# Kernel tuning notes

Hardware: AMD Instinct MI355X
Metric: run time of the kernel (lower is better)

The kernel has to match this reference:

```python
import jax, jax.numpy as jnp
import numpy as np

EPS = 1e-8  # matches torch F.cosine_similarity eps


def setup_inputs() -> dict:
    key = jax.random.key(0)
    S, U, D = 2048, 10, 256  # speakers, utterances/speaker, embedding dim
    embeddings = jax.random.normal(key, (S * U, D), dtype=jnp.float32)
    labels = jnp.repeat(jnp.arange(S, dtype=jnp.int64), U)  # speaker-blocked, as the view() assumes
    return {"embeddings": embeddings, "labels": labels}


def reference(embeddings, labels):
    labels_np = np.asarray(labels)
    S = int(np.unique(labels_np).size)          # num_speakers (static)
    B, D = embeddings.shape
    U = B // S                                   # num_utterances
    E = embeddings.reshape(S, U, D)
    C = E.mean(axis=1)                           # (S, D) centroids
    En = E / jnp.maximum(jnp.linalg.norm(E, axis=-1, keepdims=True), EPS)
    Cn = C / jnp.maximum(jnp.linalg.norm(C, axis=-1, keepdims=True), EPS)
    sim = jnp.einsum('sud,kd->suk', En, Cn)      # (S, U, S) cosine similarities
    idx = jnp.arange(S)
    pos = sim[idx, :, idx]                       # (S, U) similarity to own centroid
    neg_mask = jnp.eye(S, dtype=bool)[:, None, :]  # mask out k == i
    neg = jnp.where(neg_mask, -jnp.inf, sim)
    lse = jax.nn.logsumexp(neg, axis=-1)         # (S, U)
    loss = jnp.mean(-pos + lse)
    return loss
```

## Files before the change

### kernel.cpp

```cpp
#include <hip/hip_runtime.h>
#include <math.h>

#define SS   2048
#define UU   10
#define DD   256
#define BB   (SS * UU)
#define EPSF 1e-8f

typedef __attribute__((ext_vector_type(8))) short   bf16x8;
typedef __attribute__((ext_vector_type(4))) float   floatx4;

__device__ static inline unsigned short f2bf(float f) {
    union { float f; unsigned u; } v; v.f = f;
    unsigned r = (v.u + 0x7FFFu + ((v.u >> 16) & 1u)) >> 16;
    return (unsigned short)r;
}

__device__ static inline void gl_lds16(const unsigned short* g, unsigned short* l) {
    __builtin_amdgcn_global_load_lds((const __attribute__((address_space(1))) void*)g,
                                     (__attribute__((address_space(3))) void*)l, 16, 0, 0);
}

__global__ __launch_bounds__(256) void prep_kernel(const float* __restrict__ E,
                                                   unsigned short* __restrict__ Enb,
                                                   unsigned short* __restrict__ Cnb,
                                                   float* __restrict__ sumexp,
                                                   float* __restrict__ out) {
    const int s   = blockIdx.x;
    const int wid = threadIdx.x >> 6, lane = threadIdx.x & 63;
    __shared__ float cent[4][256];
    __shared__ float sred[256];

    if (threadIdx.x < UU) sumexp[s * UU + threadIdx.x] = 0.f;
    if (s == 0 && threadIdx.x == 0) out[0] = 0.f;

    float cp0 = 0.f, cp1 = 0.f, cp2 = 0.f, cp3 = 0.f;
    for (int u = wid; u < UU; u += 4) {
        const size_t roff = (size_t)(s * UU + u) * DD;
        float4 v = ((const float4*)(E + roff))[lane];
        float ssq = v.x * v.x + v.y * v.y + v.z * v.z + v.w * v.w;
#pragma unroll
        for (int off = 32; off; off >>= 1) ssq += __shfl_xor(ssq, off, 64);
        const float rinv = 1.0f / fmaxf(sqrtf(ssq), EPSF);
        ushort4 o;
        o.x = f2bf(v.x * rinv); o.y = f2bf(v.y * rinv);
        o.z = f2bf(v.z * rinv); o.w = f2bf(v.w * rinv);
        ((ushort4*)(Enb + roff))[lane] = o;
        cp0 += v.x; cp1 += v.y; cp2 += v.z; cp3 += v.w;
    }
    cent[wid][lane * 4 + 0] = cp0;
    cent[wid][lane * 4 + 1] = cp1;
    cent[wid][lane * 4 + 2] = cp2;
    cent[wid][lane * 4 + 3] = cp3;
    __syncthreads();

    const int d = threadIdx.x;
    const float c = (cent[0][d] + cent[1][d] + cent[2][d] + cent[3][d]) * 0.1f;
    sred[d] = c * c;
    __syncthreads();
#pragma unroll
    for (int off = 128; off; off >>= 1) {
        if (d < off) sred[d] += sred[d + off];
        __syncthreads();
    }
    const float rinv = 1.0f / fmaxf(sqrtf(sred[0]), EPSF);
    Cnb[(size_t)s * DD + d] = f2bf(c * rinv);
}

#define BM  128
#define BN  128
#define BK  32
#define NBN 2

__device__ __forceinline__ void chunk_mfma(const unsigned short* Ab,
                                           const unsigned short* Bb,
                                           const int* aoff, const int* boff,
                                           floatx4 (&acc)[4][4]) {
    bf16x8 af[4], bfr[4];
#pragma unroll
    for (int t = 0; t < 4; ++t) af[t]  = *(const bf16x8*)(Ab + aoff[t]);
#pragma unroll
    for (int t = 0; t < 4; ++t) bfr[t] = *(const bf16x8*)(Bb + boff[t]);
#pragma unroll
    for (int mt = 0; mt < 4; ++mt)
#pragma unroll
        for (int nt = 0; nt < 4; ++nt)
            acc[mt][nt] = __builtin_amdgcn_mfma_f32_16x16x32_bf16(af[mt], bfr[nt], acc[mt][nt], 0, 0, 0);
}

__global__ __launch_bounds__(256) void gemm_lse_kernel(const unsigned short* __restrict__ Enb,
                                                       const unsigned short* __restrict__ Cnb,
                                                       float* __restrict__ posArr,
                                                       float* __restrict__ sumexp) {
    __shared__ unsigned short As[BM * BK];
    __shared__ unsigned short Bs[BN * BK];

    const int tid  = threadIdx.x;
    const int wid  = tid >> 6, lane = tid & 63;
    const int l15  = lane & 15, quad = lane >> 4;
    const int wave_m = wid >> 1, wave_n = wid & 1;

    const int bm  = blockIdx.x >> 3;
    const int bnb = (blockIdx.x & 7) * NBN;
    const int row0 = bm * BM;

    const int rl = lane >> 2;
    const int gf = ((lane & 3) ^ ((rl >> 1) & 3)) * 8;
    const unsigned short* gpA[4];
    unsigned short* lp[4];
    size_t goffB[4];
#pragma unroll
    for (int i = 0; i < 4; ++i) {
        const int c = wid * 4 + i;
        if (c < 8) {
            gpA[i]  = Enb + (size_t)(row0 + c * 16 + rl) * DD + gf;
            lp[i]   = As + c * 512;
            goffB[i] = 0;
        } else {
            gpA[i]  = nullptr;
            lp[i]   = Bs + (c - 8) * 512;
            goffB[i] = (size_t)((c - 8) * 16 + rl) * DD + gf;
        }
    }

    const int fswz = (quad ^ ((l15 >> 1) & 3)) * 8;
    int aoff[4], boff[4];
#pragma unroll
    for (int t = 0; t < 4; ++t) {
        aoff[t] = (wave_m * 64 + t * 16 + l15) * BK + fswz;
        boff[t] = (wave_n * 64 + t * 16 + l15) * BK + fswz;
    }

    int lbl[4][4];
    float rs[4][4];
#pragma unroll
    for (int mt = 0; mt < 4; ++mt) {
        const int growb = row0 + wave_m * 64 + mt * 16 + quad * 4;
#pragma unroll
        for (int r = 0; r < 4; ++r) {
            lbl[mt][r] = (growb + r) / UU;
            rs[mt][r]  = 0.f;
        }
    }

    floatx4 acc[4][4];

#pragma unroll
    for (int bl = 0; bl < NBN; ++bl) {
        const int n0 = (bnb + bl) * BN;
        const unsigned short* gp[4];
#pragma unroll
        for (int i = 0; i < 4; ++i) {
            const int c = wid * 4 + i;
            gp[i] = (c < 8) ? gpA[i] : (Cnb + (size_t)n0 * DD + goffB[i]);
        }

#pragma unroll
        for (int i = 0; i < 4; ++i)
#pragma unroll
            for (int j = 0; j < 4; ++j) acc[i][j] = (floatx4){0.f, 0.f, 0.f, 0.f};

        for (int k0 = 0; k0 < DD; k0 += BK) {
            __syncthreads();
#pragma unroll
            for (int i = 0; i < 4; ++i) gl_lds16(gp[i] + k0, lp[i]);
            __syncthreads();
            chunk_mfma(As, Bs, aoff, boff, acc);
        }

#pragma unroll
        for (int mt = 0; mt < 4; ++mt) {
            const int growb = row0 + wave_m * 64 + mt * 16 + quad * 4;
#pragma unroll
            for (int nt = 0; nt < 4; ++nt) {
                const int col = n0 + wave_n * 64 + nt * 16 + l15;
#pragma unroll
                for (int r = 0; r < 4; ++r) {
                    const float sim = acc[mt][nt][r];
                    if (col == lbl[mt][r]) {
                        posArr[growb + r] = sim;
                    } else {
                        rs[mt][r] += __expf(sim);
                    }
                }
            }
        }
    }

#pragma unroll
    for (int mt = 0; mt < 4; ++mt) {
        const int growb = row0 + wave_m * 64 + mt * 16 + quad * 4;
#pragma unroll
        for (int m = 1; m < 16; m <<= 1) {
#pragma unroll
            for (int r = 0; r < 4; ++r) rs[mt][r] += __shfl_xor(rs[mt][r], m, 64);
        }
        if (l15 == 0) {
#pragma unroll
            for (int r = 0; r < 4; ++r) atomicAdd(&sumexp[growb + r], rs[mt][r]);
        }
    }
}

__global__ __launch_bounds__(256) void finalize_kernel(const float* __restrict__ posArr,
                                                       const float* __restrict__ sumexp,
                                                       float* __restrict__ out) {
    __shared__ float sred[256];
    const int tid = threadIdx.x;
    const int r = blockIdx.x * 256 + tid;
    sred[tid] = logf(sumexp[r]) - posArr[r];
    __syncthreads();
#pragma unroll
    for (int off = 128; off; off >>= 1) {
        if (tid < off) sred[tid] += sred[tid + off];
        __syncthreads();
    }
    if (tid == 0) atomicAdd(out, sred[0] * (1.0f / (float)BB));
}

extern "C" void kernel_launch(void* const* d_in, const int* in_sizes, int n_in,
                              void* d_out, int out_size, void* d_ws, size_t ws_size,
                              hipStream_t stream) {
    const float* E = (const float*)d_in[0];
    float* out = (float*)d_out;

    unsigned short* Enb = (unsigned short*)d_ws;
    unsigned short* Cnb = Enb + (size_t)BB * DD;
    float* posArr = (float*)(Cnb + (size_t)SS * DD);
    float* sumexp = posArr + BB;

    prep_kernel<<<SS, 256, 0, stream>>>(E, Enb, Cnb, sumexp, out);
    gemm_lse_kernel<<<(BB / BM) * (SS / BN / NBN), 256, 0, stream>>>(Enb, Cnb, posArr, sumexp);
    finalize_kernel<<<BB / 256, 256, 0, stream>>>(posArr, sumexp, out);
}
```

Before: 114.0 us.

## Keep full A row-tile resident in LDS and reuse across more centroid tiles

The GEMM kernel now loads the whole 128x256 bf16 embedding tile into LDS once, then streams only centroid chunks for each of four column blocks per workgroup, up from two. This halves the grid and removes repeated A reloads. Block indices are remapped with a swizzle so that neighbouring workgroups share data. The prep kernel's centroid norm reduction now uses wave shuffles instead of an LDS tree. The costs are larger LDS use per block (about 72 KB), which may lower occupancy, and fewer blocks to spread across the CUs.

```diff
diff --git a/kernel.cpp b/kernel.cpp
--- a/kernel.cpp
+++ b/kernel.cpp
@@ -29,7 +29,7 @@
     const int s   = blockIdx.x;
     const int wid = threadIdx.x >> 6, lane = threadIdx.x & 63;
     __shared__ float cent[4][256];
-    __shared__ float sred[256];
+    __shared__ float part[4];
 
     if (threadIdx.x < UU) sumexp[s * UU + threadIdx.x] = 0.f;
     if (s == 0 && threadIdx.x == 0) out[0] = 0.f;
@@ -56,21 +56,22 @@
 
     const int d = threadIdx.x;
     const float c = (cent[0][d] + cent[1][d] + cent[2][d] + cent[3][d]) * 0.1f;
-    sred[d] = c * c;
+    float p = c * c;
+#pragma unroll
+    for (int off = 32; off; off >>= 1) p += __shfl_xor(p, off, 64);
+    if (lane == 0) part[wid] = p;
     __syncthreads();
-#pragma unroll
-    for (int off = 128; off; off >>= 1) {
-        if (d < off) sred[d] += sred[d + off];
-        __syncthreads();
-    }
-    const float rinv = 1.0f / fmaxf(sqrtf(sred[0]), EPSF);
+    const float tot = part[0] + part[1] + part[2] + part[3];
+    const float rinv = 1.0f / fmaxf(sqrtf(tot), EPSF);
     Cnb[(size_t)s * DD + d] = f2bf(c * rinv);
 }
 
 #define BM  128
 #define BN  128
 #define BK  32
-#define NBN 2
+#define NCK 8
+#define NBN 4
+#define ACH (BM * BK)
 
 __device__ __forceinline__ void chunk_mfma(const unsigned short* Ab,
                                            const unsigned short* Bb,
@@ -92,7 +93,7 @@
                                                        const unsigned short* __restrict__ Cnb,
                                                        float* __restrict__ posArr,
                                                        float* __restrict__ sumexp) {
-    __shared__ unsigned short As[BM * BK];
+    __shared__ unsigned short As[NCK * ACH];
     __shared__ unsigned short Bs[BN * BK];
 
     const int tid  = threadIdx.x;
@@ -100,27 +101,21 @@
     const int l15  = lane & 15, quad = lane >> 4;
     const int wave_m = wid >> 1, wave_n = wid & 1;
 
-    const int bm  = blockIdx.x >> 3;
-    const int bnb = (blockIdx.x & 7) * NBN;
+    const int swz = (blockIdx.x & 7) * 80 + (blockIdx.x >> 3);
+    const int bm  = swz >> 2;
+    const int bnb = (swz & 3) * NBN;
     const int row0 = bm * BM;
 
     const int rl = lane >> 2;
     const int gf = ((lane & 3) ^ ((rl >> 1) & 3)) * 8;
-    const unsigned short* gpA[4];
-    unsigned short* lp[4];
-    size_t goffB[4];
-#pragma unroll
-    for (int i = 0; i < 4; ++i) {
-        const int c = wid * 4 + i;
-        if (c < 8) {
-            gpA[i]  = Enb + (size_t)(row0 + c * 16 + rl) * DD + gf;
-            lp[i]   = As + c * 512;
-            goffB[i] = 0;
-        } else {
-            gpA[i]  = nullptr;
-            lp[i]   = Bs + (c - 8) * 512;
-            goffB[i] = (size_t)((c - 8) * 16 + rl) * DD + gf;
-        }
+
+#pragma unroll 1
+    for (int j = 0; j < 16; ++j) {
+        const int id = wid * 16 + j;
+        const int k  = id >> 3;
+        const int c  = id & 7;
+        gl_lds16(Enb + (size_t)(row0 + c * 16 + rl) * DD + k * BK + gf,
+                 As + k * ACH + c * 512);
     }
 
     const int fswz = (quad ^ ((l15 >> 1) & 3)) * 8;
@@ -145,14 +140,14 @@
 
     floatx4 acc[4][4];
 
-#pragma unroll
+#pragma unroll 1
     for (int bl = 0; bl < NBN; ++bl) {
         const int n0 = (bnb + bl) * BN;
-        const unsigned short* gp[4];
-#pragma unroll
-        for (int i = 0; i < 4; ++i) {
-            const int c = wid * 4 + i;
-            gp[i] = (c < 8) ? gpA[i] : (Cnb + (size_t)n0 * DD + goffB[i]);
+        const unsigned short* gpb[2];
+#pragma unroll
+        for (int i = 0; i < 2; ++i) {
+            const int c = wid * 2 + i;
+            gpb[i] = Cnb + (size_t)(n0 + c * 16 + rl) * DD + gf;
         }
 
 #pragma unroll
@@ -160,12 +155,13 @@
 #pragma unroll
             for (int j = 0; j < 4; ++j) acc[i][j] = (floatx4){0.f, 0.f, 0.f, 0.f};
 
-        for (int k0 = 0; k0 < DD; k0 += BK) {
+        for (int k = 0; k < NCK; ++k) {
             __syncthreads();
 #pragma unroll
-            for (int i = 0; i < 4; ++i) gl_lds16(gp[i] + k0, lp[i]);
+            for (int i = 0; i < 2; ++i)
+                gl_lds16(gpb[i] + k * BK, Bs + (wid * 2 + i) * 512);
             __syncthreads();
-            chunk_mfma(As, Bs, aoff, boff, acc);
+            chunk_mfma(As + k * ACH, Bs, aoff, boff, acc);
         }
 
 #pragma unroll
```

Measured after the change: 121.4 us. +6.5%, slower.

## Process speakers per wave in prep kernel and swizzle GEMM blocks across XCDs

Applied to the files above, without the earlier changes.

The prep kernel now assigns two speakers to each wave and keeps all ten utterance rows in registers, computing row norms and the centroid with wave shuffles instead of LDS reductions and block barriers. It launches 8x fewer blocks. The GEMM block index is remapped so that blocks scheduled on the same XCD work on contiguous row/column tiles, improving L2 reuse. Higher register use per thread in prep could reduce occupancy.

```diff
diff --git a/kernel.cpp b/kernel.cpp
--- a/kernel.cpp
+++ b/kernel.cpp
@@ -26,45 +26,52 @@
                                                    unsigned short* __restrict__ Cnb,
                                                    float* __restrict__ sumexp,
                                                    float* __restrict__ out) {
-    const int s   = blockIdx.x;
     const int wid = threadIdx.x >> 6, lane = threadIdx.x & 63;
-    __shared__ float cent[4][256];
-    __shared__ float sred[256];
-
-    if (threadIdx.x < UU) sumexp[s * UU + threadIdx.x] = 0.f;
-    if (s == 0 && threadIdx.x == 0) out[0] = 0.f;
-
-    float cp0 = 0.f, cp1 = 0.f, cp2 = 0.f, cp3 = 0.f;
-    for (int u = wid; u < UU; u += 4) {
-        const size_t roff = (size_t)(s * UU + u) * DD;
-        float4 v = ((const float4*)(E + roff))[lane];
-        float ssq = v.x * v.x + v.y * v.y + v.z * v.z + v.w * v.w;
-#pragma unroll
-        for (int off = 32; off; off >>= 1) ssq += __shfl_xor(ssq, off, 64);
-        const float rinv = 1.0f / fmaxf(sqrtf(ssq), EPSF);
-        ushort4 o;
-        o.x = f2bf(v.x * rinv); o.y = f2bf(v.y * rinv);
-        o.z = f2bf(v.z * rinv); o.w = f2bf(v.w * rinv);
-        ((ushort4*)(Enb + roff))[lane] = o;
-        cp0 += v.x; cp1 += v.y; cp2 += v.z; cp3 += v.w;
-    }
-    cent[wid][lane * 4 + 0] = cp0;
-    cent[wid][lane * 4 + 1] = cp1;
-    cent[wid][lane * 4 + 2] = cp2;
-    cent[wid][lane * 4 + 3] = cp3;
-    __syncthreads();
-
-    const int d = threadIdx.x;
-    const float c = (cent[0][d] + cent[1][d] + cent[2][d] + cent[3][d]) * 0.1f;
-    sred[d] = c * c;
-    __syncthreads();
-#pragma unroll
-    for (int off = 128; off; off >>= 1) {
-        if (d < off) sred[d] += sred[d + off];
-        __syncthreads();
-    }
-    const float rinv = 1.0f / fmaxf(sqrtf(sred[0]), EPSF);
-    Cnb[(size_t)s * DD + d] = f2bf(c * rinv);
+
+    if (threadIdx.x < 80) sumexp[blockIdx.x * 80 + threadIdx.x] = 0.f;
+    if (blockIdx.x == 0 && threadIdx.x == 0) out[0] = 0.f;
+
+#pragma unroll
+    for (int sp2 = 0; sp2 < 2; ++sp2) {
+        const int sp = blockIdx.x * 8 + wid * 2 + sp2;
+        const float* rb = E + (size_t)sp * UU * DD + lane * 4;
+
+        float4 v[UU];
+#pragma unroll
+        for (int u = 0; u < UU; ++u) v[u] = *(const float4*)(rb + u * DD);
+
+        float ssq[UU];
+#pragma unroll
+        for (int u = 0; u < UU; ++u)
+            ssq[u] = v[u].x * v[u].x + v[u].y * v[u].y + v[u].z * v[u].z + v[u].w * v[u].w;
+#pragma unroll
+        for (int off = 32; off; off >>= 1) {
+#pragma unroll
+            for (int u = 0; u < UU; ++u) ssq[u] += __shfl_xor(ssq[u], off, 64);
+        }
+
+        unsigned short* eb = Enb + (size_t)sp * UU * DD + lane * 4;
+        float cx = 0.f, cy = 0.f, cz = 0.f, cw = 0.f;
+#pragma unroll
+        for (int u = 0; u < UU; ++u) {
+            const float rinv = 1.0f / fmaxf(sqrtf(ssq[u]), EPSF);
+            ushort4 o;
+            o.x = f2bf(v[u].x * rinv); o.y = f2bf(v[u].y * rinv);
+            o.z = f2bf(v[u].z * rinv); o.w = f2bf(v[u].w * rinv);
+            *(ushort4*)(eb + u * DD) = o;
+            cx += v[u].x; cy += v[u].y; cz += v[u].z; cw += v[u].w;
+        }
+
+        cx *= 0.1f; cy *= 0.1f; cz *= 0.1f; cw *= 0.1f;
+        float cs = cx * cx + cy * cy + cz * cz + cw * cw;
+#pragma unroll
+        for (int off = 32; off; off >>= 1) cs += __shfl_xor(cs, off, 64);
+        const float rinv = 1.0f / fmaxf(sqrtf(cs), EPSF);
+        ushort4 oc;
+        oc.x = f2bf(cx * rinv); oc.y = f2bf(cy * rinv);
+        oc.z = f2bf(cz * rinv); oc.w = f2bf(cw * rinv);
+        *(ushort4*)(Cnb + (size_t)sp * DD + lane * 4) = oc;
+    }
 }
 
 #define BM  128
@@ -100,8 +107,9 @@
     const int l15  = lane & 15, quad = lane >> 4;
     const int wave_m = wid >> 1, wave_n = wid & 1;
 
-    const int bm  = blockIdx.x >> 3;
-    const int bnb = (blockIdx.x & 7) * NBN;
+    const int swz = (blockIdx.x & 7) * 160 + (blockIdx.x >> 3);
+    const int bm  = swz >> 3;
+    const int bnb = (swz & 7) * NBN;
     const int row0 = bm * BM;
 
     const int rl = lane >> 2;
@@ -229,7 +237,7 @@
     float* posArr = (float*)(Cnb + (size_t)SS * DD);
     float* sumexp = posArr + BB;
 
-    prep_kernel<<<SS, 256, 0, stream>>>(E, Enb, Cnb, sumexp, out);
+    prep_kernel<<<SS / 8, 256, 0, stream>>>(E, Enb, Cnb, sumexp, out);
     gemm_lse_kernel<<<(BB / BM) * (SS / BN / NBN), 256, 0, stream>>>(Enb, Cnb, posArr, sumexp);
     finalize_kernel<<<BB / 256, 256, 0, stream>>>(posArr, sumexp, out);
 }
```

Measured after the change: 114.7 us. No clear change (+0.6%).
